# Kernel tuning notes

Measured on AMD Instinct MI355X. Metric: run time of the kernel, lower is better.

The kernel has to match this reference:

```python
import jax, jax.numpy as jnp
import numpy as np

HEADS = 8
LN_EPS = 1e-5
BN_EPS = 1e-5
MIN_EPS, MAX_EPS = 1e-4, 10.0


def _ln(x, g, b):
    m = x.mean(-1, keepdims=True)
    v = x.var(-1, keepdims=True)
    return (x - m) / jnp.sqrt(v + LN_EPS) * g + b


def _pos2d(a, b, dim, temperature=10000.0):
    # faithful to build_2d_sincos_position_embedding(w=a, h=b)
    grid_a = jnp.arange(a, dtype=jnp.float32)
    grid_b = jnp.arange(b, dtype=jnp.float32)
    ga, gb = jnp.meshgrid(grid_a, grid_b, indexing='ij')  # (a, b)
    pos_dim = dim // 4
    omega = 1.0 / (temperature ** (jnp.arange(pos_dim, dtype=jnp.float32) / pos_dim))
    out_a = ga.flatten()[:, None] * omega[None]
    out_b = gb.flatten()[:, None] * omega[None]
    return jnp.concatenate([jnp.sin(out_a), jnp.cos(out_a), jnp.sin(out_b), jnp.cos(out_b)], axis=1)  # (a*b, dim)


def _avgpool(x, k):
    bb, cc, H, W = x.shape
    return x.reshape(bb, cc, H // k, k, W // k, k).mean((3, 5))


def setup_inputs() -> dict:
    key = jax.random.key(0)
    c1, c2, bs = 256, 512, 16
    ks = jax.random.split(key, 12)

    def lin(k, o, i):
        return (jax.random.normal(k, (o, i), jnp.float32) * (1.0 / np.sqrt(i))).astype(jnp.float32)

    return {
        'a3': jax.random.normal(ks[0], (bs, c1, 80, 80), jnp.float32),
        'a4': jax.random.normal(ks[1], (bs, c2, 40, 40), jnp.float32),
        'conv_w': lin(ks[2], c1, c2), 'conv_b': jnp.zeros((c1,), jnp.float32),
        'bn_g': jnp.ones((c1,), jnp.float32), 'bn_b': jnp.zeros((c1,), jnp.float32),
        'q_w': lin(ks[3], c1, c1), 'q_b': jnp.zeros((c1,), jnp.float32),
        'q_ln_g': jnp.ones((c1,), jnp.float32), 'q_ln_b': jnp.zeros((c1,), jnp.float32),
        'k_w': lin(ks[4], c1, c1), 'k_b': jnp.zeros((c1,), jnp.float32),
        'k_ln_g': jnp.ones((c1,), jnp.float32), 'k_ln_b': jnp.zeros((c1,), jnp.float32),
        'v_w': lin(ks[5], c1, c1), 'v_b': jnp.zeros((c1,), jnp.float32),
        'out_w': lin(ks[6], c1, c1), 'out_b': jnp.zeros((c1,), jnp.float32),
        'lin1_w': lin(ks[7], 4 * c1, c1), 'lin1_b': jnp.zeros((4 * c1,), jnp.float32),
        'lin2_w': lin(ks[8], c1, 4 * c1), 'lin2_b': jnp.zeros((c1,), jnp.float32),
        'norm1_g': jnp.ones((c1,), jnp.float32), 'norm1_b': jnp.zeros((c1,), jnp.float32),
        'norm2_g': jnp.ones((c1,), jnp.float32), 'norm2_b': jnp.zeros((c1,), jnp.float32),
        'idx': 10,
    }


def reference(a3, a4, conv_w, conv_b, bn_g, bn_b, q_w, q_b, q_ln_g, q_ln_b,
              k_w, k_b, k_ln_g, k_ln_b, v_w, v_b, out_w, out_b,
              lin1_w, lin1_b, lin2_w, lin2_b, norm1_g, norm1_b, norm2_g, norm2_b, idx):
    a3 = jnp.nan_to_num(a3, nan=0.0, posinf=1e4, neginf=-1e4)
    a4 = jnp.nan_to_num(a4, nan=0.0, posinf=1e4, neginf=-1e4)
    orig_a3, orig_a4 = a3, a4

    # high_to_low_embed: 1x1 conv + BatchNorm (eval: running_mean=0, running_var=1)
    a4e = jnp.einsum('bchw,oc->bohw', a4, conv_w) + conv_b[None, :, None, None]
    a4e = a4e / jnp.sqrt(1.0 + BN_EPS) * bn_g[None, :, None, None] + bn_b[None, :, None, None]

    if idx == 10:
        a3d = _avgpool(a3, 2)
    else:
        a3d = _avgpool(a3, 4)
        a4e = _avgpool(a4e, 2)

    bs, c, h, w = a3d.shape
    tgt = h * w
    src = a4e.shape[2] * a4e.shape[3]

    residual = a3d.reshape(bs, c, tgt).transpose(0, 2, 1)      # (bs, tgt, c)
    a3f = a3d.reshape(bs, c, tgt).transpose(2, 0, 1)            # (tgt, bs, c)
    a4f = a4e.reshape(bs, c, src).transpose(2, 0, 1)            # (src, bs, c)

    pos = _pos2d(h, w, c)[:, None, :]                           # (h*w, 1, c)
    a3f = a3f + pos
    a4f = a4f + pos                                             # src == tgt by construction

    Q = jax.nn.relu(_ln(a3f @ q_w.T + q_b, q_ln_g, q_ln_b))
    K = jax.nn.relu(_ln(a4f @ k_w.T + k_b, k_ln_g, k_ln_b))
    V = a4f @ v_w.T + v_b

    hd = c // HEADS
    Q = Q.reshape(tgt, bs, HEADS, hd).transpose(1, 2, 0, 3)     # (b, h, tgt, hd)
    K = K.reshape(src, bs, HEADS, hd).transpose(1, 2, 0, 3)
    V = V.reshape(src, bs, HEADS, hd).transpose(1, 2, 0, 3)

    m = max(src, tgt)
    wi = (np.pi / 2) * jnp.arange(1, m + 1, dtype=jnp.float32) / m  # (m,)
    sq = jnp.sin(wi[:tgt])[None, None, :, None]
    cq = jnp.cos(wi[:tgt])[None, None, :, None]
    sk = jnp.sin(wi[:src])[None, None, :, None]
    ck = jnp.cos(wi[:src])[None, None, :, None]
    Q_ = jnp.concatenate([Q * sq, Q * cq], -1)                  # (b, h, tgt, 2hd)
    K_ = jnp.concatenate([K * sk, K * ck], -1)                  # (b, h, src, 2hd)

    KV = jnp.einsum('bhsd,bhse->bhde', K_, V)                   # (b, h, 2hd, hd)
    Zden = jnp.einsum('bhld,bhd->bhl', Q_, K_.sum(2))
    Z = 1.0 / jnp.clip(Zden, MIN_EPS, MAX_EPS)
    attn = jnp.einsum('bhld,bhde->bhle', Q_, KV) * Z[..., None]  # (b, h, tgt, hd)

    attn = attn.transpose(2, 0, 1, 3).reshape(tgt, bs, c)
    out = (attn @ out_w.T + out_b).transpose(1, 0, 2)           # (bs, tgt, c)
    out = _ln(out, norm1_g, norm1_b)
    out = residual + out

    res2 = out
    ff = jax.nn.gelu(out @ lin1_w.T + lin1_b, approximate=False) @ lin2_w.T + lin2_b
    ff = _ln(ff, norm2_g, norm2_b)
    out = res2 + ff

    a3_sa = out.transpose(0, 2, 1).reshape(bs, c, h, w)
    a3_sa = jax.image.resize(a3_sa, orig_a3.shape, 'bilinear')  # align_corners=False
    a3_sa = a3_sa * orig_a3

    B4, C4, H4, W4 = orig_a4.shape
    a4_up = jax.image.resize(orig_a4, (B4, C4, 2 * H4, 2 * W4), 'bilinear')
    return (a3_sa, a4_up)
```

## Files before the change

### kernel.cpp

```cpp
#include <hip/hip_runtime.h>
#include <math.h>


typedef __attribute__((ext_vector_type(8))) short bf16x8;
typedef __attribute__((ext_vector_type(8))) unsigned short us8;
typedef __attribute__((ext_vector_type(4))) unsigned short us4h;
typedef __attribute__((ext_vector_type(4))) float f32x4;

__device__ __forceinline__ unsigned short f2bf(float f) {
  unsigned int u = __float_as_uint(f);
  u += 0x7fff + ((u >> 16) & 1);
  return (unsigned short)(u >> 16);
}
__device__ __forceinline__ float bf2f(unsigned short u) {
  return __uint_as_float(((unsigned int)u) << 16);
}

__global__ __launch_bounds__(256) void wprep_kernel(
    const float* __restrict__ cw, const float* __restrict__ qw,
    const float* __restrict__ kw, const float* __restrict__ vw,
    const float* __restrict__ ow, const float* __restrict__ l1w,
    const float* __restrict__ l2w, unsigned short* __restrict__ wbf) {
  int gid = blockIdx.x * 256 + threadIdx.x;
  size_t e0 = (size_t)gid * 8;
  const float* src; size_t off;
  if (e0 < 131072)      { src = cw;  off = e0; }
  else if (e0 < 196608) { src = qw;  off = e0 - 131072; }
  else if (e0 < 262144) { src = kw;  off = e0 - 196608; }
  else if (e0 < 327680) { src = vw;  off = e0 - 262144; }
  else if (e0 < 393216) { src = ow;  off = e0 - 327680; }
  else if (e0 < 655360) { src = l1w; off = e0 - 393216; }
  else                  { src = l2w; off = e0 - 655360; }
  float4 v0 = *(const float4*)(src + off);
  float4 v1 = *(const float4*)(src + off + 4);
  us8 r;
  r[0] = f2bf(v0.x); r[1] = f2bf(v0.y); r[2] = f2bf(v0.z); r[3] = f2bf(v0.w);
  r[4] = f2bf(v1.x); r[5] = f2bf(v1.y); r[6] = f2bf(v1.z); r[7] = f2bf(v1.w);
  *(us8*)(wbf + e0) = r;
}

__global__ void pos_kernel(float* __restrict__ pos) {
  int s = blockIdx.x, c = threadIdx.x;
  int y = s / 40, x = s - y * 40;
  int quad = c >> 6, i = c & 63;
  float omega = expf(-(float)i * (9.2103403719761836f / 64.0f));
  float coord = (quad < 2) ? (float)y : (float)x;
  float a = coord * omega;
  pos[s * 256 + c] = (quad & 1) ? cosf(a) : sinf(a);
}

__global__ __launch_bounds__(640) void avgpool_kernel(
    const float* __restrict__ a3, const float* __restrict__ pos,
    unsigned short* __restrict__ X3) {
  __shared__ float buf2[256][44];
  int y = blockIdx.x, b = blockIdx.y;
  int tid = threadIdx.x;
  int x2 = tid % 20, cq = tid / 20;
#pragma unroll
  for (int it = 0; it < 8; ++it) {
    int c = cq + 32 * it;
    const float* p = a3 + (((size_t)(b * 256 + c) * 80 + 2 * y) * 80 + x2 * 4);
    float4 r0 = *(const float4*)p;
    float4 r1 = *(const float4*)(p + 80);
    buf2[c][2 * x2]     = 0.25f * ((r0.x + r0.y) + (r1.x + r1.y));
    buf2[c][2 * x2 + 1] = 0.25f * ((r0.z + r0.w) + (r1.z + r1.w));
  }
  __syncthreads();
  size_t t0 = (size_t)b * 1600 + y * 40;
  int sbase = y * 40;
#pragma unroll
  for (int it = 0; it < 4; ++it) {
    int idx = it * 640 + tid;
    int c = idx & 255, xq = idx >> 8;
    int x0 = xq * 4;
    float4 v = *(const float4*)&buf2[c][x0];
#pragma unroll
    for (int j = 0; j < 4; ++j) {
      float pv = pos[(size_t)(sbase + x0 + j) * 256 + c];
      float vv = (j == 0) ? v.x : (j == 1) ? v.y : (j == 2) ? v.z : v.w;
      X3[(t0 + x0 + j) * 256 + c] = f2bf(vv + pv);
    }
  }
}

__global__ __launch_bounds__(256) void a4t_kernel(
    const float* __restrict__ a4, unsigned short* __restrict__ a4t) {
  __shared__ float buf[64][65];
  int s0 = blockIdx.x * 64, k0 = blockIdx.y * 64, b = blockIdx.z;
  const float* src = a4 + ((size_t)b * 512 + k0) * 1600 + s0;
#pragma unroll
  for (int p = 0; p < 4; ++p) {
    int idx = p * 256 + threadIdx.x;
    int kk = idx >> 4, s4 = (idx & 15) * 4;
    float4 v = *(const float4*)(src + (size_t)kk * 1600 + s4);
    buf[kk][s4 + 0] = v.x; buf[kk][s4 + 1] = v.y;
    buf[kk][s4 + 2] = v.z; buf[kk][s4 + 3] = v.w;
  }
  __syncthreads();
  unsigned short* dst = a4t + ((size_t)b * 1600 + s0) * 512 + k0;
#pragma unroll
  for (int p = 0; p < 4; ++p) {
    int idx = p * 256 + threadIdx.x;
    int ss = idx >> 4, kq = (idx & 15) * 4;
    us4h v;
    v[0] = f2bf(buf[kq + 0][ss]); v[1] = f2bf(buf[kq + 1][ss]);
    v[2] = f2bf(buf[kq + 2][ss]); v[3] = f2bf(buf[kq + 3][ss]);
    *(us4h*)(dst + (size_t)ss * 512 + kq) = v;
  }
}

template<int EPI>
__global__ __launch_bounds__(256) void fgemm(
    const unsigned short* __restrict__ A, const unsigned short* __restrict__ W,
    const float* __restrict__ bias, void* __restrict__ outp,
    const int K, const int ldN,
    const float* __restrict__ posb,
    const float* __restrict__ g1, const float* __restrict__ b1,
    const unsigned short* __restrict__ res) {
  __shared__ __align__(16) unsigned short Albs[64][40];
  __shared__ __align__(16) unsigned short Wlds[256][40];
  __shared__ float part[2][64][2];
  int tid = threadIdx.x;
  int lane = tid & 63, w = tid >> 6;
  int m0 = (w >> 1) * 32, n0 = (w & 1) * 128;
  int g = lane >> 4, cl = lane & 15;
  int t0 = blockIdx.x * 64, o0 = blockIdx.y * 256;
  f32x4 acc[2][8] = {};
  int arr = tid >> 2, acol = (tid & 3) * 8;

  for (int k0 = 0; k0 < K; k0 += 32) {
    __syncthreads();
    *(us8*)&Albs[arr][acol] = *(const us8*)(A + (size_t)(t0 + arr) * K + (k0 + acol));
#pragma unroll
    for (int p = 0; p < 4; ++p) {
      int idx = p * 256 + tid;
      int rr = idx >> 2, cc = (idx & 3) * 8;
      *(us8*)&Wlds[rr][cc] = *(const us8*)(W + (size_t)(o0 + rr) * K + (k0 + cc));
    }
    __syncthreads();
    bf16x8 af[2], bw[8];
#pragma unroll
    for (int ms = 0; ms < 2; ++ms)
      af[ms] = *(const bf16x8*)&Albs[m0 + ms * 16 + cl][g * 8];
#pragma unroll
    for (int ns = 0; ns < 8; ++ns)
      bw[ns] = *(const bf16x8*)&Wlds[n0 + ns * 16 + cl][g * 8];
#pragma unroll
    for (int ms = 0; ms < 2; ++ms)
#pragma unroll
      for (int ns = 0; ns < 8; ++ns)
        acc[ms][ns] = __builtin_amdgcn_mfma_f32_16x16x32_bf16(af[ms], bw[ns], acc[ms][ns], 0, 0, 0);
  }

  float bv[8];
#pragma unroll
  for (int ns = 0; ns < 8; ++ns) bv[ns] = bias[o0 + n0 + ns * 16 + cl];
  int sbase = t0 % 1600;

  if constexpr (EPI == 2 || EPI == 3 || EPI == 5) {
#pragma unroll
    for (int ms = 0; ms < 2; ++ms) {
#pragma unroll
      for (int i = 0; i < 4; ++i) {
        float p = 0.f, q = 0.f;
#pragma unroll
        for (int ns = 0; ns < 8; ++ns) {
          float v = acc[ms][ns][i] + bv[ns];
          p += v; q += v * v;
        }
        p += __shfl_xor(p, 1); q += __shfl_xor(q, 1);
        p += __shfl_xor(p, 2); q += __shfl_xor(q, 2);
        p += __shfl_xor(p, 4); q += __shfl_xor(q, 4);
        p += __shfl_xor(p, 8); q += __shfl_xor(q, 8);
        if (cl == 0) {
          int rl = m0 + ms * 16 + g * 4 + i;
          part[w & 1][rl][0] = p;
          part[w & 1][rl][1] = q;
        }
      }
    }
    __syncthreads();
  }

  unsigned short* ob = (unsigned short*)outp;
  float* of = (float*)outp;
#pragma unroll
  for (int ms = 0; ms < 2; ++ms) {
#pragma unroll
    for (int i = 0; i < 4; ++i) {
      int rl = m0 + ms * 16 + g * 4 + i;
      int t = t0 + rl;
      float mean = 0.f, inv = 0.f;
      if constexpr (EPI == 2 || EPI == 3 || EPI == 5) {
        float sp = part[0][rl][0] + part[1][rl][0];
        float sq = part[0][rl][1] + part[1][rl][1];
        mean = sp * (1.f / 256.f);
        float var = sq * (1.f / 256.f) - mean * mean;
        inv = rsqrtf(var + 1e-5f);
      }
#pragma unroll
      for (int ns = 0; ns < 8; ++ns) {
        int col = n0 + ns * 16 + cl;
        float v = acc[ms][ns][i] + bv[ns];
        size_t oidx = (size_t)t * ldN + o0 + col;
        if constexpr (EPI == 0) {
          ob[oidx] = f2bf(v);
        } else if constexpr (EPI == 1) {
          const float is = 0.99999500003749968f;
          float y = v * (is * g1[col]) + b1[col] + posb[(size_t)(sbase + rl) * 256 + col];
          ob[oidx] = f2bf(y);
        } else if constexpr (EPI == 2) {
          float y = (v - mean) * inv * g1[col] + b1[col];
          ob[oidx] = f2bf(fmaxf(y, 0.f));
        } else if constexpr (EPI == 3) {
          float y = (v - mean) * inv * g1[col] + b1[col];
          y += bf2f(res[(size_t)t * 256 + col]) - posb[(size_t)(sbase + rl) * 256 + col];
          ob[oidx] = f2bf(y);
        } else if constexpr (EPI == 4) {
          float y = 0.5f * v * (1.f + erff(v * 0.7071067811865475f));
          ob[oidx] = f2bf(y);
        } else {
          float y = (v - mean) * inv * g1[col] + b1[col];
          y += bf2f(res[(size_t)t * 256 + col]);
          of[oidx] = y;
        }
      }
    }
  }
}

__global__ __launch_bounds__(256) void kv_kernel(
    const unsigned short* __restrict__ Kb, const unsigned short* __restrict__ Vb,
    float* __restrict__ KVp, float* __restrict__ Ksp) {
  __shared__ float Kc[64][32];
  __shared__ float Vc[64][32];
  __shared__ float sv[64], cv[64];
  __shared__ float red[4][64];
  int bx = blockIdx.x;
  int bh = bx / 5, sp = bx - bh * 5;
  int b = bh >> 3, h = bh & 7;
  int tid = threadIdx.x;
  int e = tid & 31, dg = tid >> 5;
  int d4 = dg * 4;
  int dks = tid & 63, partid = tid >> 6;
  float accs[4] = {0.f, 0.f, 0.f, 0.f};
  float accc[4] = {0.f, 0.f, 0.f, 0.f};
  float ks = 0.f;
  size_t base = ((size_t)b * 1600) * 256 + h * 32;
  for (int s0 = sp * 320; s0 < sp * 320 + 320; s0 += 64) {
    __syncthreads();
#pragma unroll
    for (int p = 0; p < 8; ++p) {
      int si = dg + p * 8;
      Kc[si][e] = bf2f(Kb[base + (size_t)(s0 + si) * 256 + e]);
      Vc[si][e] = bf2f(Vb[base + (size_t)(s0 + si) * 256 + e]);
    }
    if (tid < 64) {
      float wv = 1.5707963267948966f * (float)(s0 + tid + 1) * (1.0f / 1600.0f);
      sv[tid] = sinf(wv);
      cv[tid] = cosf(wv);
    }
    __syncthreads();
#pragma unroll 8
    for (int si = 0; si < 64; ++si) {
      float vv = Vc[si][e];
      float sn = sv[si], cs = cv[si];
      float4 k4 = *(const float4*)&Kc[si][d4];
      float p0 = k4.x * vv, p1 = k4.y * vv, p2 = k4.z * vv, p3 = k4.w * vv;
      accs[0] = fmaf(p0, sn, accs[0]); accc[0] = fmaf(p0, cs, accc[0]);
      accs[1] = fmaf(p1, sn, accs[1]); accc[1] = fmaf(p1, cs, accc[1]);
      accs[2] = fmaf(p2, sn, accs[2]); accc[2] = fmaf(p2, cs, accc[2]);
      accs[3] = fmaf(p3, sn, accs[3]); accc[3] = fmaf(p3, cs, accc[3]);
    }
#pragma unroll 4
    for (int q = 0; q < 16; ++q) {
      int si = partid * 16 + q;
      float kvv = (dks < 32) ? Kc[si][dks] * sv[si] : Kc[si][dks - 32] * cv[si];
      ks += kvv;
    }
  }
  red[partid][dks] = ks;
  __syncthreads();
  size_t ob = (size_t)sp * 128 + bh;
  if (tid < 64)
    Ksp[ob * 64 + tid] = (red[0][tid] + red[1][tid]) + (red[2][tid] + red[3][tid]);
#pragma unroll
  for (int i = 0; i < 4; ++i) {
    KVp[ob * 2048 + (d4 + i) * 32 + e] = accs[i];
    KVp[ob * 2048 + (32 + d4 + i) * 32 + e] = accc[i];
  }
}

__global__ __launch_bounds__(256) void kvred_kernel(
    const float* __restrict__ KVp, const float* __restrict__ Ksp,
    float* __restrict__ KV, float* __restrict__ Ks) {
  int bh = blockIdx.x, tid = threadIdx.x;
  size_t o = (size_t)bh * 2048 + tid * 8;
  float4 s0 = make_float4(0, 0, 0, 0), s1 = make_float4(0, 0, 0, 0);
#pragma unroll
  for (int sp = 0; sp < 5; ++sp) {
    const float* p = KVp + ((size_t)sp * 128 + bh) * 2048 + tid * 8;
    float4 a = *(const float4*)p;
    float4 b2 = *(const float4*)(p + 4);
    s0.x += a.x; s0.y += a.y; s0.z += a.z; s0.w += a.w;
    s1.x += b2.x; s1.y += b2.y; s1.z += b2.z; s1.w += b2.w;
  }
  *(float4*)(KV + o) = s0;
  *(float4*)(KV + o + 4) = s1;
  if (tid < 64) {
    float t = 0.f;
#pragma unroll
    for (int sp = 0; sp < 5; ++sp) t += Ksp[((size_t)sp * 128 + bh) * 64 + tid];
    Ks[bh * 64 + tid] = t;
  }
}

__global__ __launch_bounds__(256) void attn_kernel(
    const unsigned short* __restrict__ Qb, const float* __restrict__ KV,
    const float* __restrict__ Ksum, unsigned short* __restrict__ attn) {
  int grp = threadIdx.x >> 5;
  int e = threadIdx.x & 31;
  int t = blockIdx.x * 8 + grp;
  int b = t / 1600, s = t - b * 1600;
  float wv = 1.5707963267948966f * (float)(s + 1) * (1.0f / 1600.0f);
  float sq = sinf(wv), cq = cosf(wv);
  const unsigned short* qrow = Qb + (size_t)t * 256;
  for (int h = 0; h < 8; ++h) {
    int bh = b * 8 + h;
    const float* kv = KV + (size_t)bh * 2048;
    const float* ksm = Ksum + (size_t)bh * 64;
    float qe = bf2f(qrow[h * 32 + e]);
    float zp = qe * (sq * ksm[e] + cq * ksm[32 + e]);
    zp += __shfl_xor(zp, 1); zp += __shfl_xor(zp, 2);
    zp += __shfl_xor(zp, 4); zp += __shfl_xor(zp, 8); zp += __shfl_xor(zp, 16);
    float acc = 0.f;
#pragma unroll 8
    for (int d = 0; d < 32; ++d) {
      float qv = bf2f(qrow[h * 32 + d]);
      acc = fmaf(qv * sq, kv[d * 32 + e], acc);
      acc = fmaf(qv * cq, kv[(32 + d) * 32 + e], acc);
    }
    float zc = fminf(fmaxf(zp, 1e-4f), 10.0f);
    attn[(size_t)t * 256 + h * 32 + e] = f2bf(acc * (1.0f / zc));
  }
}

__global__ __launch_bounds__(256) void transpose_kernel(
    const float* __restrict__ X, float* __restrict__ Y) {
  __shared__ float buf[40 * 257];
  int y = blockIdx.x, b = blockIdx.y;
  int tid = threadIdx.x;
  size_t t0 = (size_t)b * 1600 + y * 40;
  for (int it = 0; it < 40; ++it)
    buf[it * 257 + tid] = X[(t0 + it) * 256 + tid];
  __syncthreads();
  for (int it = 0; it < 40; ++it) {
    int idx = it * 256 + tid;
    int c = idx / 40, x = idx - c * 40;
    Y[((size_t)(b * 256 + c) * 1600) + y * 40 + x] = buf[x * 257 + c];
  }
}

__device__ __forceinline__ float bilin40(const float* sm, int Y, int X) {
  float fy = Y * 0.5f - 0.25f;
  int iy = (int)floorf(fy);
  float dy = fy - (float)iy;
  int y0 = iy < 0 ? 0 : iy;
  int y1 = (iy + 1) > 39 ? 39 : (iy + 1);
  float fx = X * 0.5f - 0.25f;
  int ix = (int)floorf(fx);
  float dx = fx - (float)ix;
  int x0 = ix < 0 ? 0 : ix;
  int x1 = (ix + 1) > 39 ? 39 : (ix + 1);
  float v00 = sm[y0 * 40 + x0], v01 = sm[y0 * 40 + x1];
  float v10 = sm[y1 * 40 + x0], v11 = sm[y1 * 40 + x1];
  return (1.f - dy) * ((1.f - dx) * v00 + dx * v01) +
         dy * ((1.f - dx) * v10 + dx * v11);
}

__global__ __launch_bounds__(256) void upsample_mul_kernel(
    const float* __restrict__ src, const float* __restrict__ a3, float* __restrict__ out) {
  __shared__ float sm[1600];
  int c = blockIdx.x, b = blockIdx.y;
  size_t sbase = ((size_t)b * 256 + c) * 1600;
  for (int i = threadIdx.x; i < 1600; i += 256) sm[i] = src[sbase + i];
  __syncthreads();
  size_t obase = ((size_t)b * 256 + c) * 6400;
  for (int it = 0; it < 25; ++it) {
    int idx = it * 256 + threadIdx.x;
    int Y = idx / 80, X = idx - Y * 80;
    out[obase + idx] = bilin40(sm, Y, X) * a3[obase + idx];
  }
}

__global__ __launch_bounds__(256) void upsample_kernel(
    const float* __restrict__ src, float* __restrict__ out) {
  __shared__ float sm[1600];
  int c = blockIdx.x, b = blockIdx.y;
  size_t sbase = ((size_t)b * 512 + c) * 1600;
  for (int i = threadIdx.x; i < 1600; i += 256) sm[i] = src[sbase + i];
  __syncthreads();
  size_t obase = ((size_t)b * 512 + c) * 6400;
  for (int it = 0; it < 25; ++it) {
    int idx = it * 256 + threadIdx.x;
    int Y = idx / 80, X = idx - Y * 80;
    out[obase + idx] = bilin40(sm, Y, X);
  }
}

extern "C" void kernel_launch(void* const* d_in, const int* in_sizes, int n_in,
                              void* d_out, int out_size, void* d_ws, size_t ws_size,
                              hipStream_t stream) {
  const float* a3     = (const float*)d_in[0];
  const float* a4     = (const float*)d_in[1];
  const float* conv_w = (const float*)d_in[2];
  const float* conv_b = (const float*)d_in[3];
  const float* bn_g   = (const float*)d_in[4];
  const float* bn_b   = (const float*)d_in[5];
  const float* q_w    = (const float*)d_in[6];
  const float* q_b    = (const float*)d_in[7];
  const float* q_ln_g = (const float*)d_in[8];
  const float* q_ln_b = (const float*)d_in[9];
  const float* k_w    = (const float*)d_in[10];
  const float* k_b    = (const float*)d_in[11];
  const float* k_ln_g = (const float*)d_in[12];
  const float* k_ln_b = (const float*)d_in[13];
  const float* v_w    = (const float*)d_in[14];
  const float* v_b    = (const float*)d_in[15];
  const float* out_w  = (const float*)d_in[16];
  const float* out_b  = (const float*)d_in[17];
  const float* lin1_w = (const float*)d_in[18];
  const float* lin1_b = (const float*)d_in[19];
  const float* lin2_w = (const float*)d_in[20];
  const float* lin2_b = (const float*)d_in[21];
  const float* n1_g   = (const float*)d_in[22];
  const float* n1_b   = (const float*)d_in[23];
  const float* n2_g   = (const float*)d_in[24];
  const float* n2_b   = (const float*)d_in[25];
  (void)in_sizes; (void)n_in; (void)out_size; (void)ws_size;

  float* ws = (float*)d_ws;
  float* pos  = ws + 0;
  unsigned short* wbf = (unsigned short*)(ws + 409600);
  float* KV   = ws + 868352;
  float* Ks   = ws + 1130496;
  float* KVp  = ws + 1138688;
  float* Ksp  = ws + 2449408;
  unsigned short* X3b  = (unsigned short*)(ws + 2490368);
  unsigned short* X4b  = (unsigned short*)(ws + 5767168);
  unsigned short* Qbb  = (unsigned short*)(ws + 9043968);
  unsigned short* Kbb  = (unsigned short*)(ws + 12320768);
  unsigned short* Vbb  = (unsigned short*)(ws + 15597568);
  unsigned short* o1b  = (unsigned short*)(ws + 18874368);
  unsigned short* a4tb = (unsigned short*)(ws + 22151168);
  unsigned short* ffhb = (unsigned short*)(ws + 22151168);
  float* out2 = ws + 9043968;
  float* a3p  = ws + 15597568;

  const unsigned short* w_conv = wbf;
  const unsigned short* w_q    = wbf + 131072;
  const unsigned short* w_k    = wbf + 196608;
  const unsigned short* w_v    = wbf + 262144;
  const unsigned short* w_o    = wbf + 327680;
  const unsigned short* w_l1   = wbf + 393216;
  const unsigned short* w_l2   = wbf + 655360;

  float* out0 = (float*)d_out;
  float* out1f = out0 + (size_t)16 * 256 * 80 * 80;

  wprep_kernel<<<448, 256, 0, stream>>>(conv_w, q_w, k_w, v_w, out_w, lin1_w, lin2_w, wbf);
  pos_kernel<<<1600, 256, 0, stream>>>(pos);
  avgpool_kernel<<<dim3(40, 16), 640, 0, stream>>>(a3, pos, X3b);
  a4t_kernel<<<dim3(25, 8, 16), 256, 0, stream>>>(a4, a4tb);
  fgemm<1><<<dim3(400, 1), 256, 0, stream>>>(a4tb, w_conv, conv_b, X4b, 512, 256, pos, bn_g, bn_b, nullptr);
  fgemm<2><<<dim3(400, 1), 256, 0, stream>>>(X3b, w_q, q_b, Qbb, 256, 256, nullptr, q_ln_g, q_ln_b, nullptr);
  fgemm<2><<<dim3(400, 1), 256, 0, stream>>>(X4b, w_k, k_b, Kbb, 256, 256, nullptr, k_ln_g, k_ln_b, nullptr);
  fgemm<0><<<dim3(400, 1), 256, 0, stream>>>(X4b, w_v, v_b, Vbb, 256, 256, nullptr, nullptr, nullptr, nullptr);
  kv_kernel<<<640, 256, 0, stream>>>(Kbb, Vbb, KVp, Ksp);
  kvred_kernel<<<128, 256, 0, stream>>>(KVp, Ksp, KV, Ks);
  attn_kernel<<<3200, 256, 0, stream>>>(Qbb, KV, Ks, Kbb );
  fgemm<3><<<dim3(400, 1), 256, 0, stream>>>(Kbb, w_o, out_b, o1b, 256, 256, pos, n1_g, n1_b, X3b);
  fgemm<4><<<dim3(400, 4), 256, 0, stream>>>(o1b, w_l1, lin1_b, ffhb, 256, 1024, nullptr, nullptr, nullptr, nullptr);
  fgemm<5><<<dim3(400, 1), 256, 0, stream>>>(ffhb, w_l2, lin2_b, out2, 1024, 256, nullptr, n2_g, n2_b, o1b);
  transpose_kernel<<<dim3(40, 16), 256, 0, stream>>>(out2, a3p);
  upsample_mul_kernel<<<dim3(256, 16), 256, 0, stream>>>(a3p, a3, out0);
  upsample_kernel<<<dim3(512, 16), 256, 0, stream>>>(a4, out1f);
}
```

Baseline: 455.2 us.

## Fuse transpose into final GEMM epilogue and vectorize bilinear upsampling

```diff
diff --git a/kernel.cpp b/kernel.cpp
--- a/kernel.cpp
+++ b/kernel.cpp
@@ -182,8 +182,41 @@
     __syncthreads();
   }
 
+  if constexpr (EPI == 5) {
+    float* of = (float*)outp;
+    int bb = t0 / 1600;
+#pragma unroll
+    for (int ms = 0; ms < 2; ++ms) {
+      int rl0 = m0 + ms * 16 + g * 4;
+      float mean[4], inv[4];
+#pragma unroll
+      for (int i = 0; i < 4; ++i) {
+        float sp = part[0][rl0 + i][0] + part[1][rl0 + i][0];
+        float sq = part[0][rl0 + i][1] + part[1][rl0 + i][1];
+        mean[i] = sp * (1.f / 256.f);
+        float var = sq * (1.f / 256.f) - mean[i] * mean[i];
+        inv[i] = rsqrtf(var + 1e-5f);
+      }
+#pragma unroll
+      for (int ns = 0; ns < 8; ++ns) {
+        int col = n0 + ns * 16 + cl;
+        float gg = g1[col], b2 = b1[col];
+        float4 y;
+#pragma unroll
+        for (int i = 0; i < 4; ++i) {
+          float v = acc[ms][ns][i] + bv[ns];
+          float yy = (v - mean[i]) * inv[i] * gg + b2;
+          yy += bf2f(res[(size_t)(t0 + rl0 + i) * 256 + col]);
+          if (i == 0) y.x = yy; else if (i == 1) y.y = yy;
+          else if (i == 2) y.z = yy; else y.w = yy;
+        }
+        *(float4*)(of + ((size_t)(bb * 256 + col) * 1600) + sbase + rl0) = y;
+      }
+    }
+    return;
+  }
+
   unsigned short* ob = (unsigned short*)outp;
-  float* of = (float*)outp;
 #pragma unroll
   for (int ms = 0; ms < 2; ++ms) {
 #pragma unroll
@@ -191,7 +224,7 @@
       int rl = m0 + ms * 16 + g * 4 + i;
       int t = t0 + rl;
       float mean = 0.f, inv = 0.f;
-      if constexpr (EPI == 2 || EPI == 3 || EPI == 5) {
+      if constexpr (EPI == 2 || EPI == 3) {
         float sp = part[0][rl][0] + part[1][rl][0];
         float sq = part[0][rl][1] + part[1][rl][1];
         mean = sp * (1.f / 256.f);
@@ -219,10 +252,6 @@
         } else if constexpr (EPI == 4) {
           float y = 0.5f * v * (1.f + erff(v * 0.7071067811865475f));
           ob[oidx] = f2bf(y);
-        } else {
-          float y = (v - mean) * inv * g1[col] + b1[col];
-          y += bf2f(res[(size_t)t * 256 + col]);
-          of[oidx] = y;
         }
       }
     }
@@ -345,37 +374,27 @@
   }
 }
 
-__global__ __launch_bounds__(256) void transpose_kernel(
-    const float* __restrict__ X, float* __restrict__ Y) {
-  __shared__ float buf[40 * 257];
-  int y = blockIdx.x, b = blockIdx.y;
-  int tid = threadIdx.x;
-  size_t t0 = (size_t)b * 1600 + y * 40;
-  for (int it = 0; it < 40; ++it)
-    buf[it * 257 + tid] = X[(t0 + it) * 256 + tid];
-  __syncthreads();
-  for (int it = 0; it < 40; ++it) {
-    int idx = it * 256 + tid;
-    int c = idx / 40, x = idx - c * 40;
-    Y[((size_t)(b * 256 + c) * 1600) + y * 40 + x] = buf[x * 257 + c];
-  }
-}
-
-__device__ __forceinline__ float bilin40(const float* sm, int Y, int X) {
+__device__ __forceinline__ float4 up_row4(const float* sm, int Y, int q) {
   float fy = Y * 0.5f - 0.25f;
   int iy = (int)floorf(fy);
   float dy = fy - (float)iy;
   int y0 = iy < 0 ? 0 : iy;
   int y1 = (iy + 1) > 39 ? 39 : (iy + 1);
-  float fx = X * 0.5f - 0.25f;
-  int ix = (int)floorf(fx);
-  float dx = fx - (float)ix;
-  int x0 = ix < 0 ? 0 : ix;
-  int x1 = (ix + 1) > 39 ? 39 : (ix + 1);
-  float v00 = sm[y0 * 40 + x0], v01 = sm[y0 * 40 + x1];
-  float v10 = sm[y1 * 40 + x0], v11 = sm[y1 * 40 + x1];
-  return (1.f - dy) * ((1.f - dx) * v00 + dx * v01) +
-         dy * ((1.f - dx) * v10 + dx * v11);
+  const float* r0 = sm + y0 * 40;
+  const float* r1 = sm + y1 * 40;
+  int cm1 = (2 * q - 1) < 0 ? 0 : (2 * q - 1);
+  int cp2 = (2 * q + 2) > 39 ? 39 : (2 * q + 2);
+  float w1 = 1.f - dy;
+  float s0 = w1 * r0[cm1]       + dy * r1[cm1];
+  float s1 = w1 * r0[2 * q]     + dy * r1[2 * q];
+  float s2 = w1 * r0[2 * q + 1] + dy * r1[2 * q + 1];
+  float s3 = w1 * r0[cp2]       + dy * r1[cp2];
+  float4 o;
+  o.x = 0.25f * s0 + 0.75f * s1;
+  o.y = 0.75f * s1 + 0.25f * s2;
+  o.z = 0.25f * s1 + 0.75f * s2;
+  o.w = 0.75f * s2 + 0.25f * s3;
+  return o;
 }
 
 __global__ __launch_bounds__(256) void upsample_mul_kernel(
@@ -383,13 +402,16 @@
   __shared__ float sm[1600];
   int c = blockIdx.x, b = blockIdx.y;
   size_t sbase = ((size_t)b * 256 + c) * 1600;
-  for (int i = threadIdx.x; i < 1600; i += 256) sm[i] = src[sbase + i];
+  for (int i = threadIdx.x; i < 400; i += 256)
+    *(float4*)&sm[i * 4] = *(const float4*)(src + sbase + i * 4);
   __syncthreads();
   size_t obase = ((size_t)b * 256 + c) * 6400;
-  for (int it = 0; it < 25; ++it) {
-    int idx = it * 256 + threadIdx.x;
-    int Y = idx / 80, X = idx - Y * 80;
-    out[obase + idx] = bilin40(sm, Y, X) * a3[obase + idx];
+  for (int i = threadIdx.x; i < 1600; i += 256) {
+    int Y = i / 20, q = i - Y * 20;
+    float4 o = up_row4(sm, Y, q);
+    float4 m = *(const float4*)(a3 + obase + i * 4);
+    o.x *= m.x; o.y *= m.y; o.z *= m.z; o.w *= m.w;
+    *(float4*)(out + obase + i * 4) = o;
   }
 }
 
@@ -398,13 +420,14 @@
   __shared__ float sm[1600];
   int c = blockIdx.x, b = blockIdx.y;
   size_t sbase = ((size_t)b * 512 + c) * 1600;
-  for (int i = threadIdx.x; i < 1600; i += 256) sm[i] = src[sbase + i];
+  for (int i = threadIdx.x; i < 400; i += 256)
+    *(float4*)&sm[i * 4] = *(const float4*)(src + sbase + i * 4);
   __syncthreads();
   size_t obase = ((size_t)b * 512 + c) * 6400;
-  for (int it = 0; it < 25; ++it) {
-    int idx = it * 256 + threadIdx.x;
-    int Y = idx / 80, X = idx - Y * 80;
-    out[obase + idx] = bilin40(sm, Y, X);
+  for (int i = threadIdx.x; i < 1600; i += 256) {
+    int Y = i / 20, q = i - Y * 20;
+    float4 o = up_row4(sm, Y, q);
+    *(float4*)(out + obase + i * 4) = o;
   }
 }
 
@@ -454,8 +477,7 @@
   unsigned short* o1b  = (unsigned short*)(ws + 18874368);
   unsigned short* a4tb = (unsigned short*)(ws + 22151168);
   unsigned short* ffhb = (unsigned short*)(ws + 22151168);
-  float* out2 = ws + 9043968;
-  float* a3p  = ws + 15597568;
+  float* a3p  = ws + 9043968;
 
   const unsigned short* w_conv = wbf;
   const unsigned short* w_q    = wbf + 131072;
@@ -481,8 +503,7 @@
   attn_kernel<<<3200, 256, 0, stream>>>(Qbb, KV, Ks, Kbb );
   fgemm<3><<<dim3(400, 1), 256, 0, stream>>>(Kbb, w_o, out_b, o1b, 256, 256, pos, n1_g, n1_b, X3b);
   fgemm<4><<<dim3(400, 4), 256, 0, stream>>>(o1b, w_l1, lin1_b, ffhb, 256, 1024, nullptr, nullptr, nullptr, nullptr);
-  fgemm<5><<<dim3(400, 1), 256, 0, stream>>>(ffhb, w_l2, lin2_b, out2, 1024, 256, nullptr, n2_g, n2_b, o1b);
-  transpose_kernel<<<dim3(40, 16), 256, 0, stream>>>(out2, a3p);
+  fgemm<5><<<dim3(400, 1), 256, 0, stream>>>(ffhb, w_l2, lin2_b, a3p, 1024, 256, nullptr, n2_g, n2_b, o1b);
   upsample_mul_kernel<<<dim3(256, 16), 256, 0, stream>>>(a3p, a3, out0);
   upsample_kernel<<<dim3(512, 16), 256, 0, stream>>>(a4, out1f);
 }
```

Result: no change. 453.9 us (-0.3%).
